# Kernel optimization log

Measured on AMD Instinct MI355X. Metric: run time of the kernel, lower is better.

Reference implementation:

```python
import jax, jax.numpy as jnp
import numpy as np

N = 50000   # nodes
D = 128     # input_dim
E = 1600000 # edges
K = 100     # out_nodes


def setup_inputs() -> dict:
    key = jax.random.key(0)
    ks = jax.random.split(key, 9)
    x = jax.random.normal(ks[0], (N, D), dtype=jnp.float32)
    edge_index = jax.random.randint(ks[1], (2, E), 0, N, dtype=jnp.int64)
    # PyG GCNConv params: Linear(in,out,bias=False) weight + separate bias
    s = 1.0 / np.sqrt(D)
    W1 = jax.random.uniform(ks[2], (D, D), jnp.float32, -s, s)
    b1 = jnp.zeros((D,), jnp.float32)
    W2 = jax.random.uniform(ks[3], (D, D), jnp.float32, -s, s)
    b2 = jnp.zeros((D,), jnp.float32)
    Wa = jax.random.uniform(ks[4], (D, K), jnp.float32, -s, s)
    ba = jax.random.uniform(ks[5], (K,), jnp.float32, -s, s)
    return {"x": x, "edge_index": edge_index, "W1": W1, "b1": b1,
            "W2": W2, "b2": b2, "Wa": Wa, "ba": ba}


def _gcn_conv(x, src, dst, norm, W, b, n_nodes):
    # PyG GCNConv: h = x @ W; aggregate D^-1/2 (A+I) D^-1/2 h; add bias
    h = x @ W                                  # [N, D]
    msg = h[src] * norm[:, None]               # [E+N, D] gather + scale
    agg = jax.ops.segment_sum(msg, dst, num_segments=n_nodes)  # scatter-add
    return agg + b


def reference(x, edge_index, W1, b1, W2, b2, Wa, ba):
    n = x.shape[0]
    loop = jnp.arange(n, dtype=edge_index.dtype)
    src = jnp.concatenate([edge_index[0], loop])   # add self-loops
    dst = jnp.concatenate([edge_index[1], loop])
    deg = jnp.zeros((n,), x.dtype).at[dst].add(1.0)
    dinv = jnp.where(deg > 0, jax.lax.rsqrt(deg), 0.0)
    norm = dinv[src] * dinv[dst]                   # [E+N]

    h = _gcn_conv(x, src, dst, norm, W1, b1, n)
    h = jax.nn.relu(h)
    h = _gcn_conv(h, src, dst, norm, W2, b2, n)
    s = jax.nn.softmax(h @ Wa + ba, axis=1)        # [N, K]
    return s
```

## Files before the change

kernel.cpp:

```cpp
#include <hip/hip_runtime.h>

#define D 128
#define KOUT 100
#define CHUNK 4096

typedef __attribute__((ext_vector_type(8))) short short8;
typedef __attribute__((ext_vector_type(4))) float floatx4;

__device__ inline float bf_lo(unsigned int u) { return __uint_as_float(u << 16); }
__device__ inline float bf_hi(unsigned int u) { return __uint_as_float(u & 0xFFFF0000u); }

__device__ inline unsigned int bf_round(float a) {
    unsigned int ua = __float_as_uint(a);
    return (ua + 0x7FFFu + ((ua >> 16) & 1u)) >> 16;
}
__device__ inline unsigned int pack_bf(float a, float b) {
    return bf_round(a) | (bf_round(b) << 16);
}

__device__ void gemm_body(const void* __restrict__ Xin, const unsigned short* __restrict__ Wf,
                          const float* __restrict__ bias, const int* __restrict__ deg,
                          void* __restrict__ Y, int nrows, int in_bf16, int out_mode,
                          float* lds_f, int tile) {
    unsigned short* lds_h = (unsigned short*)lds_f;
    unsigned int* lds_u = (unsigned int*)lds_f;

    int tid = threadIdx.x;
    int w = tid >> 6, lane = tid & 63;
    int quad = lane >> 4, m16 = lane & 15;
    int r0 = tile * 64;

    if (!in_bf16) {
        int row = tid >> 2, cg_ = tid & 3;
        bool valid = (r0 + row) < nrows;
        const float4* Xr = (const float4*)Xin + (size_t)(r0 + row) * 32 + cg_ * 8;
#pragma unroll
        for (int j = 0; j < 8; j++) {
            float4 v = valid ? Xr[j] : make_float4(0.f, 0.f, 0.f, 0.f);
            int c = cg_ * 32 + j * 4;
            lds_u[row * 68 + (c >> 1)]     = pack_bf(v.x, v.y);
            lds_u[row * 68 + (c >> 1) + 1] = pack_bf(v.z, v.w);
        }
        __syncthreads();
    }

    floatx4 acc[8];
#pragma unroll
    for (int ct = 0; ct < 8; ct++) acc[ct] = (floatx4){0.f, 0.f, 0.f, 0.f};

    int arow = r0 + w * 16 + m16;
    if (arow > nrows - 1) arow = nrows - 1;
    const unsigned int* Xb = (const unsigned int*)Xin;

    const short8* Wf8 = (const short8*)Wf;
#pragma unroll
    for (int kt = 0; kt < 4; kt++) {
        short8 a;
        if (in_bf16) {
            a = *(const short8*)(Xb + (size_t)arow * 64 + kt * 16 + quad * 4);
        } else {
            a = *(const short8*)(lds_h + (w * 16 + m16) * 136 + kt * 32 + quad * 8);
        }
#pragma unroll
        for (int ct = 0; ct < 8; ct++) {
            short8 b = Wf8[(kt * 8 + ct) * 64 + lane];
            acc[ct] = __builtin_amdgcn_mfma_f32_16x16x32_bf16(a, b, acc[ct], 0, 0, 0);
        }
    }

    if (out_mode == 1) {
        __syncthreads();
#pragma unroll
        for (int ct = 0; ct < 8; ct++) {
#pragma unroll
            for (int r = 0; r < 4; r++) {
                int rl = w * 16 + quad * 4 + r;
                lds_f[rl * 130 + ct * 16 + m16] = acc[ct][r];
            }
        }
        __syncthreads();
        unsigned int* Yb = (unsigned int*)Y;
        for (int r = 0; r < 16; r++) {
            int row = r0 + w * 16 + r;
            if (row < nrows) {
                float sc = deg ? rsqrtf((float)(deg[row] + 1)) : 1.f;
                float lo = lds_f[(w * 16 + r) * 130 + 2 * lane] * sc;
                float hi = lds_f[(w * 16 + r) * 130 + 2 * lane + 1] * sc;
                Yb[(size_t)row * 64 + lane] = pack_bf(lo, hi);
            }
        }
    } else {
        float bb[8];
#pragma unroll
        for (int ct = 0; ct < 8; ct++) bb[ct] = bias[ct * 16 + m16];
        float* Yf = (float*)Y;
#pragma unroll
        for (int r = 0; r < 4; r++) {
            int row = r0 + w * 16 + quad * 4 + r;
            float vv[8];
            float mx = -1e30f;
#pragma unroll
            for (int ct = 0; ct < 8; ct++) {
                int col = ct * 16 + m16;
                vv[ct] = (col < KOUT) ? acc[ct][r] + bb[ct] : -1e30f;
                mx = fmaxf(mx, vv[ct]);
            }
#pragma unroll
            for (int off = 1; off < 16; off <<= 1) mx = fmaxf(mx, __shfl_xor(mx, off));
            float se = 0.f;
#pragma unroll
            for (int ct = 0; ct < 8; ct++) {
                vv[ct] = (vv[ct] > -1e29f) ? __expf(vv[ct] - mx) : 0.f;
                se += vv[ct];
            }
#pragma unroll
            for (int off = 1; off < 16; off <<= 1) se += __shfl_xor(se, off);
            float inv = 1.f / se;
            if (row < nrows) {
#pragma unroll
                for (int ct = 0; ct < 8; ct++) {
                    int col = ct * 16 + m16;
                    if (col < KOUT) Yf[(size_t)row * KOUT + col] = vv[ct] * inv;
                }
            }
        }
    }
}


__launch_bounds__(256)
__global__ void k_p1_prep(const int* __restrict__ ei, int E, int nbuck, int cap,
                          int* __restrict__ bcur, unsigned int* __restrict__ bdata,
                          int* __restrict__ deg,
                          const float* __restrict__ W1, const float* __restrict__ W2,
                          const float* __restrict__ Wa, const float* __restrict__ ba,
                          const float* __restrict__ b2,
                          unsigned short* __restrict__ Wf1, unsigned short* __restrict__ WfF,
                          float* __restrict__ bpad, int* __restrict__ rowptr,
                          unsigned int* __restrict__ zrowA, unsigned int* __restrict__ zrowB,
                          int n, int nbP1) {
    __shared__ float lds_f[64 * 130];
    int tid = threadIdx.x;

    if ((int)blockIdx.x < nbP1) {
        int* hist = (int*)lds_f;
        int* sc   = hist + 256;
        int* pfx  = sc + 256;
        int* cur  = pfx + 256;
        int* gbase = cur + 256;
        unsigned int* lbuf = (unsigned int*)(gbase + 256);
        unsigned char* bkt = (unsigned char*)(lbuf + CHUNK);

        int base = blockIdx.x * CHUNK;
        int cnt = E - base; if (cnt > CHUNK) cnt = CHUNK;

        hist[tid] = 0;
        __syncthreads();

        int src[CHUNK / 256];
        int dst[CHUNK / 256];
#pragma unroll
        for (int q = 0; q < CHUNK / 256; q++) {
            int li = tid + q * 256;
            if (li < cnt) {
                src[q] = ei[base + li];
                dst[q] = ei[E + base + li];
                atomicAdd(&hist[dst[q] >> 8], 1);
            }
        }
        __syncthreads();

        int v = hist[tid];
        sc[tid] = v;
        __syncthreads();
        for (int off = 1; off < 256; off <<= 1) {
            int t = (tid >= off) ? sc[tid - off] : 0;
            __syncthreads();
            sc[tid] += t;
            __syncthreads();
        }
        int excl = sc[tid] - v;
        pfx[tid] = excl;
        cur[tid] = excl;
        gbase[tid] = 0;
        if (tid < nbuck && v > 0) gbase[tid] = atomicAdd(&bcur[tid], v);
        __syncthreads();

#pragma unroll
        for (int q = 0; q < CHUNK / 256; q++) {
            int li = tid + q * 256;
            if (li < cnt) {
                int b = dst[q] >> 8;
                int p = atomicAdd(&cur[b], 1);
                lbuf[p] = (unsigned int)src[q] | ((unsigned int)(dst[q] & 255) << 24);
                bkt[p] = (unsigned char)b;
            }
        }
        __syncthreads();

        for (int p = tid; p < cnt; p += 256) {
            int b = bkt[p];
            unsigned int rec = lbuf[p];
            bdata[(size_t)b * cap + gbase[b] + (p - pfx[b])] = rec;
            atomicAdd(deg + b * 256 + (int)(rec >> 24), 1);
        }
    } else {
        int idx = ((int)blockIdx.x - nbP1) * 256 + tid;
        if (idx < 2 * 16384) {
            int m = idx >> 14;
            int e = idx & 16383;
            int j = e & 7, lane = (e >> 3) & 63, ct = (e >> 9) & 7, kt = e >> 12;
            int k = kt * 32 + (lane >> 4) * 8 + j;
            int col = ct * 16 + (lane & 15);
            if (m == 0) {
                Wf1[e] = (unsigned short)bf_round(W1[k * 128 + col]);
            } else {
                float s = 0.f;
                if (col < KOUT) {
                    const float* w2r = W2 + k * 128;
#pragma unroll 8
                    for (int mm = 0; mm < 128; mm++)
                        s = fmaf(w2r[mm], Wa[mm * KOUT + col], s);
                }
                WfF[e] = (unsigned short)bf_round(s);
            }
        }
        if (idx < 128) {
            float s = 0.f;
            if (idx < KOUT) {
                for (int mm = 0; mm < 128; mm++)
                    s = fmaf(b2[mm], Wa[mm * KOUT + idx], s);
                s += ba[idx];
            }
            bpad[idx] = s;
        }
        if (idx < 64) { zrowA[idx] = 0u; zrowB[idx] = 0u; }
        if (idx == 64) rowptr[n] = E;
    }
}


__launch_bounds__(256)
__global__ void k_build_gemm(const unsigned int* __restrict__ bdata, const int* __restrict__ bcur,
                             int cap, int* __restrict__ rowptr, int* __restrict__ csr,
                             int n, int nbuck,
                             const float* __restrict__ X, const unsigned short* __restrict__ Wf1,
                             const int* __restrict__ deg, unsigned int* __restrict__ HbA) {
    __shared__ float lds_f[64 * 130];
    int tid = threadIdx.x;

    if ((int)blockIdx.x < nbuck) {
        int* cnts = (int*)lds_f;
        int* sc   = cnts + 256;
        int* cur  = sc + 256;
        int* pbb  = cur + 256;

        int b = blockIdx.x;
        if (tid == 0) pbb[0] = 0;
        cnts[tid] = 0;
        __syncthreads();

        int part = 0;
        for (int t = tid; t < b; t += 256) part += bcur[t];
#pragma unroll
        for (int off = 32; off > 0; off >>= 1) part += __shfl_down(part, off);
        if ((tid & 63) == 0 && part != 0) atomicAdd(&pbb[0], part);

        int cnt = bcur[b];
        const unsigned int* p = bdata + (size_t)b * cap;
        for (int e = tid; e < cnt; e += 256) atomicAdd(&cnts[p[e] >> 24], 1);
        __syncthreads();

        int v = cnts[tid];
        sc[tid] = v;
        __syncthreads();
        for (int off = 1; off < 256; off <<= 1) {
            int t = (tid >= off) ? sc[tid - off] : 0;
            __syncthreads();
            sc[tid] += t;
            __syncthreads();
        }
        int gstart = pbb[0] + (sc[tid] - v);
        int node = b * 256 + tid;
        if (node < n) rowptr[node] = gstart;
        cur[tid] = gstart;
        __syncthreads();

        for (int e = tid; e < cnt; e += 256) {
            unsigned int u = p[e];
            int pos = atomicAdd(&cur[u >> 24], 1);
            csr[pos] = (int)(u & 0xFFFFFFu);
        }
    } else {
        gemm_body(X, Wf1, nullptr, deg, HbA, n, 0, 1, lds_f, (int)blockIdx.x - nbuck);
    }
}

__launch_bounds__(256)
__global__ void k_gemm_final(const void* __restrict__ Xin, const unsigned short* __restrict__ WfF,
                             const float* __restrict__ bpad, void* __restrict__ out, int n) {
    __shared__ float lds_f[64 * 130];
    gemm_body(Xin, WfF, bpad, nullptr, out, n, 1, 2, lds_f, (int)blockIdx.x);
}


__launch_bounds__(256)
__global__ void aggregate_kernel(const uint4* __restrict__ Hb4, const int* __restrict__ csr,
                                 const int* __restrict__ rowptr,
                                 const float* __restrict__ bias,
                                 unsigned int* __restrict__ Ob, int n, int do_relu, int post_scale) {
    int wid = threadIdx.x >> 6, lane = threadIdx.x & 63;
    int g = lane >> 4, c = lane & 15;
    int i = blockIdx.x * 4 + wid;
    if (i >= n) return;

    int start = rowptr[i];
    int cnt = rowptr[i + 1] - start;
    const int* cp = csr + start;
    float di = rsqrtf((float)(cnt + 1));

    float acc[8];
    {
        uint4 sv = Hb4[(size_t)i * 16 + c];
        unsigned int su[4] = {sv.x, sv.y, sv.z, sv.w};
        if (g != 0) { su[0] = su[1] = su[2] = su[3] = 0u; }
#pragma unroll
        for (int t = 0; t < 4; t++) {
            acc[2 * t]     = bf_lo(su[t]);
            acc[2 * t + 1] = bf_hi(su[t]);
        }
    }

    int s[4];
#pragma unroll
    for (int u = 0; u < 4; u++) {
        int idx = u * 4 + g;
        s[u] = (idx < cnt) ? cp[idx] : n;
    }
    for (int e = 0; e < cnt; e += 16) {
        uint4 v[4];
#pragma unroll
        for (int u = 0; u < 4; u++) v[u] = Hb4[(size_t)s[u] * 16 + c];
        int ns[4];
#pragma unroll
        for (int u = 0; u < 4; u++) {
            int idx = e + 16 + u * 4 + g;
            ns[u] = (idx < cnt) ? cp[idx] : n;
        }
#pragma unroll
        for (int u = 0; u < 4; u++) {
            unsigned int uu[4] = {v[u].x, v[u].y, v[u].z, v[u].w};
#pragma unroll
            for (int t = 0; t < 4; t++) {
                acc[2 * t]     += bf_lo(uu[t]);
                acc[2 * t + 1] += bf_hi(uu[t]);
            }
        }
#pragma unroll
        for (int u = 0; u < 4; u++) s[u] = ns[u];
    }

#pragma unroll
    for (int j = 0; j < 8; j++) {
        acc[j] += __shfl_xor(acc[j], 16);
        acc[j] += __shfl_xor(acc[j], 32);
    }

    float2 bb = bias ? ((const float2*)bias)[c * 4 + g] : make_float2(0.f, 0.f);
    float fx = acc[g * 2]     * di + bb.x;
    float fy = acc[g * 2 + 1] * di + bb.y;
    if (do_relu) { fx = fmaxf(fx, 0.f); fy = fmaxf(fy, 0.f); }
    if (post_scale) { fx *= di; fy *= di; }
    Ob[(size_t)i * 64 + c * 4 + g] = pack_bf(fx, fy);
}


extern "C" void kernel_launch(void* const* d_in, const int* in_sizes, int n_in,
                              void* d_out, int out_size, void* d_ws, size_t ws_size,
                              hipStream_t stream) {
    const float* x  = (const float*)d_in[0];
    const int*   ei = (const int*)d_in[1];
    const float* W1 = (const float*)d_in[2];
    const float* b1 = (const float*)d_in[3];
    const float* W2 = (const float*)d_in[4];
    const float* b2 = (const float*)d_in[5];
    const float* Wa = (const float*)d_in[6];
    const float* ba = (const float*)d_in[7];
    float* out = (float*)d_out;

    int N = in_sizes[0] / D;
    int E = in_sizes[1] / 2;

    int nbuck = (N + 255) >> 8;
    int cap = ((E / nbuck) + 2048 + 63) & ~63;

    char* w = (char*)d_ws;
    size_t off = 0;
    auto carve = [&](size_t bytes) -> void* {
        void* p = w + off;
        off = (off + bytes + 255) & ~(size_t)255;
        return p;
    };
    int*   bcur   = (int*)carve(256 * 4);
    int*   deg    = (int*)carve((size_t)N * 4);
    int*   rowptr = (int*)carve((size_t)(N + 1) * 4);
    unsigned int* bdata = (unsigned int*)carve((size_t)nbuck * cap * 4);
    int*   csr    = (int*)carve((size_t)E * 4);
    unsigned short* Wf1 = (unsigned short*)carve(16384 * 2);
    unsigned short* WfF = (unsigned short*)carve(16384 * 2);
    float* bpad   = (float*)carve(512);
    unsigned int* HbA = (unsigned int*)carve((size_t)(N + 1) * 64 * 4);
    unsigned int* HbB = (unsigned int*)carve((size_t)(N + 1) * 64 * 4);
    (void)ws_size; (void)n_in; (void)out_size;

    int nbNode4 = (N + 3) / 4;
    int nbGemm = (N + 63) / 64;
    int nbP1 = (E + CHUNK - 1) / CHUNK;

    (void)hipMemsetAsync(bcur, 0, 1024 + (size_t)N * 4, stream);

    k_p1_prep<<<nbP1 + 128, 256, 0, stream>>>(ei, E, nbuck, cap, bcur, bdata, deg,
                                              W1, W2, Wa, ba, b2, Wf1, WfF, bpad, rowptr,
                                              HbA + (size_t)N * 64, HbB + (size_t)N * 64,
                                              N, nbP1);
    k_build_gemm<<<nbuck + nbGemm, 256, 0, stream>>>(bdata, bcur, cap, rowptr, csr, N, nbuck,
                                                     x, Wf1, deg, HbA);
    aggregate_kernel<<<nbNode4, 256, 0, stream>>>((const uint4*)HbA, csr, rowptr, b1, HbB, N, 1, 1);
    aggregate_kernel<<<nbNode4, 256, 0, stream>>>((const uint4*)HbB, csr, rowptr, nullptr, HbA, N, 0, 0);
    k_gemm_final<<<nbGemm, 256, 0, stream>>>(HbA, WfF, bpad, out, N);
}
```

Measured before the change: 273.6 us.

## Compute dinv from CSR row counts and scale per-edge in aggregation

Stops computing node degrees with global atomics in the bucketing pass. dinv is now derived from the per-node counts already available while building the CSR, and the D^-1/2 source-side scaling moves from the GEMM output and post-scale into a per-edge FMA inside the aggregation loop. This removes 1.6M scattered atomics and shrinks the memset. The cost is an extra gather of dinv[src] per edge in both aggregation passes.

```diff
diff --git a/kernel.cpp b/kernel.cpp
--- a/kernel.cpp
+++ b/kernel.cpp
@@ -19,7 +19,7 @@
 }
 
 __device__ void gemm_body(const void* __restrict__ Xin, const unsigned short* __restrict__ Wf,
-                          const float* __restrict__ bias, const int* __restrict__ deg,
+                          const float* __restrict__ bias,
                           void* __restrict__ Y, int nrows, int in_bf16, int out_mode,
                           float* lds_f, int tile) {
     unsigned short* lds_h = (unsigned short*)lds_f;
@@ -83,9 +83,8 @@
         for (int r = 0; r < 16; r++) {
             int row = r0 + w * 16 + r;
             if (row < nrows) {
-                float sc = deg ? rsqrtf((float)(deg[row] + 1)) : 1.f;
-                float lo = lds_f[(w * 16 + r) * 130 + 2 * lane] * sc;
-                float hi = lds_f[(w * 16 + r) * 130 + 2 * lane + 1] * sc;
+                float lo = lds_f[(w * 16 + r) * 130 + 2 * lane];
+                float hi = lds_f[(w * 16 + r) * 130 + 2 * lane + 1];
                 Yb[(size_t)row * 64 + lane] = pack_bf(lo, hi);
             }
         }
@@ -131,12 +130,12 @@
 __launch_bounds__(256)
 __global__ void k_p1_prep(const int* __restrict__ ei, int E, int nbuck, int cap,
                           int* __restrict__ bcur, unsigned int* __restrict__ bdata,
-                          int* __restrict__ deg,
                           const float* __restrict__ W1, const float* __restrict__ W2,
                           const float* __restrict__ Wa, const float* __restrict__ ba,
                           const float* __restrict__ b2,
                           unsigned short* __restrict__ Wf1, unsigned short* __restrict__ WfF,
                           float* __restrict__ bpad, int* __restrict__ rowptr,
+                          float* __restrict__ dinv,
                           unsigned int* __restrict__ zrowA, unsigned int* __restrict__ zrowB,
                           int n, int nbP1) {
     __shared__ float lds_f[64 * 130];
@@ -200,9 +199,7 @@
 
         for (int p = tid; p < cnt; p += 256) {
             int b = bkt[p];
-            unsigned int rec = lbuf[p];
-            bdata[(size_t)b * cap + gbase[b] + (p - pfx[b])] = rec;
-            atomicAdd(deg + b * 256 + (int)(rec >> 24), 1);
+            bdata[(size_t)b * cap + gbase[b] + (p - pfx[b])] = lbuf[p];
         }
     } else {
         int idx = ((int)blockIdx.x - nbP1) * 256 + tid;
@@ -236,16 +233,18 @@
         }
         if (idx < 64) { zrowA[idx] = 0u; zrowB[idx] = 0u; }
         if (idx == 64) rowptr[n] = E;
+        if (idx == 65) dinv[n] = 0.f;
     }
 }
 
 
 __launch_bounds__(256)
 __global__ void k_build_gemm(const unsigned int* __restrict__ bdata, const int* __restrict__ bcur,
-                             int cap, int* __restrict__ rowptr, int* __restrict__ csr,
+                             int cap, float* __restrict__ dinv,
+                             int* __restrict__ rowptr, int* __restrict__ csr,
                              int n, int nbuck,
                              const float* __restrict__ X, const unsigned short* __restrict__ Wf1,
-                             const int* __restrict__ deg, unsigned int* __restrict__ HbA) {
+                             unsigned int* __restrict__ HbA) {
     __shared__ float lds_f[64 * 130];
     int tid = threadIdx.x;
 
@@ -282,7 +281,10 @@
         }
         int gstart = pbb[0] + (sc[tid] - v);
         int node = b * 256 + tid;
-        if (node < n) rowptr[node] = gstart;
+        if (node < n) {
+            dinv[node] = rsqrtf((float)(v + 1));
+            rowptr[node] = gstart;
+        }
         cur[tid] = gstart;
         __syncthreads();
 
@@ -292,7 +294,7 @@
             csr[pos] = (int)(u & 0xFFFFFFu);
         }
     } else {
-        gemm_body(X, Wf1, nullptr, deg, HbA, n, 0, 1, lds_f, (int)blockIdx.x - nbuck);
+        gemm_body(X, Wf1, nullptr, HbA, n, 0, 1, lds_f, (int)blockIdx.x - nbuck);
     }
 }
 
@@ -300,15 +302,15 @@
 __global__ void k_gemm_final(const void* __restrict__ Xin, const unsigned short* __restrict__ WfF,
                              const float* __restrict__ bpad, void* __restrict__ out, int n) {
     __shared__ float lds_f[64 * 130];
-    gemm_body(Xin, WfF, bpad, nullptr, out, n, 1, 2, lds_f, (int)blockIdx.x);
+    gemm_body(Xin, WfF, bpad, out, n, 1, 2, lds_f, (int)blockIdx.x);
 }
 
 
 __launch_bounds__(256)
 __global__ void aggregate_kernel(const uint4* __restrict__ Hb4, const int* __restrict__ csr,
-                                 const int* __restrict__ rowptr,
+                                 const int* __restrict__ rowptr, const float* __restrict__ dinv,
                                  const float* __restrict__ bias,
-                                 unsigned int* __restrict__ Ob, int n, int do_relu, int post_scale) {
+                                 unsigned int* __restrict__ Ob, int n, int do_relu) {
     int wid = threadIdx.x >> 6, lane = threadIdx.x & 63;
     int g = lane >> 4, c = lane & 15;
     int i = blockIdx.x * 4 + wid;
@@ -326,17 +328,21 @@
         if (g != 0) { su[0] = su[1] = su[2] = su[3] = 0u; }
 #pragma unroll
         for (int t = 0; t < 4; t++) {
-            acc[2 * t]     = bf_lo(su[t]);
-            acc[2 * t + 1] = bf_hi(su[t]);
+            acc[2 * t]     = di * bf_lo(su[t]);
+            acc[2 * t + 1] = di * bf_hi(su[t]);
         }
     }
 
     int s[4];
+    float dv[4];
 #pragma unroll
     for (int u = 0; u < 4; u++) {
         int idx = u * 4 + g;
         s[u] = (idx < cnt) ? cp[idx] : n;
     }
+#pragma unroll
+    for (int u = 0; u < 4; u++) dv[u] = dinv[s[u]];
+
     for (int e = 0; e < cnt; e += 16) {
         uint4 v[4];
 #pragma unroll
@@ -347,17 +353,20 @@
             int idx = e + 16 + u * 4 + g;
             ns[u] = (idx < cnt) ? cp[idx] : n;
         }
+        float ndv[4];
+#pragma unroll
+        for (int u = 0; u < 4; u++) ndv[u] = dinv[ns[u]];
 #pragma unroll
         for (int u = 0; u < 4; u++) {
             unsigned int uu[4] = {v[u].x, v[u].y, v[u].z, v[u].w};
 #pragma unroll
             for (int t = 0; t < 4; t++) {
-                acc[2 * t]     += bf_lo(uu[t]);
-                acc[2 * t + 1] += bf_hi(uu[t]);
-            }
-        }
-#pragma unroll
-        for (int u = 0; u < 4; u++) s[u] = ns[u];
+                acc[2 * t]     = fmaf(dv[u], bf_lo(uu[t]), acc[2 * t]);
+                acc[2 * t + 1] = fmaf(dv[u], bf_hi(uu[t]), acc[2 * t + 1]);
+            }
+        }
+#pragma unroll
+        for (int u = 0; u < 4; u++) { s[u] = ns[u]; dv[u] = ndv[u]; }
     }
 
 #pragma unroll
@@ -370,7 +379,6 @@
     float fx = acc[g * 2]     * di + bb.x;
     float fy = acc[g * 2 + 1] * di + bb.y;
     if (do_relu) { fx = fmaxf(fx, 0.f); fy = fmaxf(fy, 0.f); }
-    if (post_scale) { fx *= di; fy *= di; }
     Ob[(size_t)i * 64 + c * 4 + g] = pack_bf(fx, fy);
 }
 
@@ -402,7 +410,7 @@
         return p;
     };
     int*   bcur   = (int*)carve(256 * 4);
-    int*   deg    = (int*)carve((size_t)N * 4);
+    float* dinv   = (float*)carve((size_t)(N + 1) * 4);
     int*   rowptr = (int*)carve((size_t)(N + 1) * 4);
     unsigned int* bdata = (unsigned int*)carve((size_t)nbuck * cap * 4);
     int*   csr    = (int*)carve((size_t)E * 4);
@@ -417,15 +425,16 @@
     int nbGemm = (N + 63) / 64;
     int nbP1 = (E + CHUNK - 1) / CHUNK;
 
-    (void)hipMemsetAsync(bcur, 0, 1024 + (size_t)N * 4, stream);
-
-    k_p1_prep<<<nbP1 + 128, 256, 0, stream>>>(ei, E, nbuck, cap, bcur, bdata, deg,
-                                              W1, W2, Wa, ba, b2, Wf1, WfF, bpad, rowptr,
+    (void)hipMemsetAsync(bcur, 0, 256 * 4, stream);
+
+    k_p1_prep<<<nbP1 + 128, 256, 0, stream>>>(ei, E, nbuck, cap, bcur, bdata,
+                                              W1, W2, Wa, ba, b2, Wf1, WfF, bpad,
+                                              rowptr, dinv,
                                               HbA + (size_t)N * 64, HbB + (size_t)N * 64,
                                               N, nbP1);
-    k_build_gemm<<<nbuck + nbGemm, 256, 0, stream>>>(bdata, bcur, cap, rowptr, csr, N, nbuck,
-                                                     x, Wf1, deg, HbA);
-    aggregate_kernel<<<nbNode4, 256, 0, stream>>>((const uint4*)HbA, csr, rowptr, b1, HbB, N, 1, 1);
-    aggregate_kernel<<<nbNode4, 256, 0, stream>>>((const uint4*)HbB, csr, rowptr, nullptr, HbA, N, 0, 0);
+    k_build_gemm<<<nbuck + nbGemm, 256, 0, stream>>>(bdata, bcur, cap, dinv, rowptr, csr,
+                                                     N, nbuck, x, Wf1, HbA);
+    aggregate_kernel<<<nbNode4, 256, 0, stream>>>((const uint4*)HbA, csr, rowptr, dinv, b1, HbB, N, 1);
+    aggregate_kernel<<<nbNode4, 256, 0, stream>>>((const uint4*)HbB, csr, rowptr, dinv, nullptr, HbA, N, 0);
     k_gemm_final<<<nbGemm, 256, 0, stream>>>(HbA, WfF, bpad, out, N);
 }
```

Result: faster. 241.7 us (-11.6%).
